# Optimization experiments

Measured on AMD Instinct MI355X. Metric: run time of the kernel, lower is better.

The kernel has to match this reference:

```python
import jax, jax.numpy as jnp
import numpy as np

BLOCK_H, BLOCK_W = 8, 8
IMG_H, IMG_W = 256, 512
NBLOCKS = 256
NSEQ = 256
BATCH = 16
TILES = (IMG_H // BLOCK_H) * (IMG_W // BLOCK_W)  # 2048
TAU = 1.0


def gen_deblocking_lut():
    l = np.zeros((3, 3, 3), np.float32)
    l[2, 0, 0] = 1.0
    l[1, 0, 1] = 1.0; l[2, 0, 1] = 2.0
    l[0, 0, 2] = 1.0; l[1, 0, 2] = 1.0; l[2, 0, 2] = 2.0
    l[1, 1, 0] = 1.0; l[2, 1, 0] = 2.0
    l[0, 1, 1] = 1.0; l[1, 1, 1] = 1.0; l[2, 1, 1] = 2.0
    l[0, 1, 2] = 1.0; l[1, 1, 2] = 2.0; l[2, 1, 2] = 2.0
    l[0, 2, 0] = 1.0; l[1, 2, 0] = 1.0; l[2, 2, 0] = 2.0
    l[0, 2, 1] = 1.0; l[1, 2, 1] = 2.0; l[2, 2, 1] = 2.0
    l[0, 2, 2] = 1.0; l[1, 2, 2] = 2.0; l[2, 2, 2] = 2.0
    return jnp.asarray(l)


def trilinear_interp(lut, x, y, z):
    # lut: (3,3,3); x,y,z: same shape, floats (indices clamped like torch version)
    x0 = jnp.clip(jnp.floor(x), 0, 1).astype(jnp.int32)
    y0 = jnp.clip(jnp.floor(y), 0, 1).astype(jnp.int32)
    z0 = jnp.clip(jnp.floor(z), 0, 1).astype(jnp.int32)
    x1 = jnp.clip(x0 + 1, 0, 2)
    y1 = jnp.clip(y0 + 1, 0, 2)
    z1 = jnp.clip(z0 + 1, 0, 2)
    xd = x - x0.astype(x.dtype)
    yd = y - y0.astype(y.dtype)
    zd = z - z0.astype(z.dtype)
    c000 = lut[x0, y0, z0]; c100 = lut[x1, y0, z0]
    c010 = lut[x0, y1, z0]; c110 = lut[x1, y1, z0]
    c001 = lut[x0, y0, z1]; c101 = lut[x1, y0, z1]
    c011 = lut[x0, y1, z1]; c111 = lut[x1, y1, z1]
    c00 = c000 * (1 - xd) * (1 - yd) + c100 * xd * (1 - yd) + c010 * (1 - xd) * yd + c110 * xd * yd
    c01 = c001 * (1 - xd) * (1 - yd) + c101 * xd * (1 - yd) + c011 * (1 - xd) * yd + c111 * xd * yd
    return c00 * (1 - zd) + c01 * zd


def deblocking_filter(img_raw, lut):
    # Faithful port, including the source quirks: second pass reuses `center`
    # (pre-filter image) in the LUT lookup and shifts along W, not H.
    img = img_raw * 2
    B, C, H, W = img.shape
    xm = jnp.arange(W) % BLOCK_W
    ym = jnp.arange(H) % BLOCK_H
    mask_x = ((xm == 0) | (xm == BLOCK_W - 1)).reshape(1, 1, 1, W)
    mask_y = ((ym == 0) | (ym == BLOCK_H - 1)).reshape(1, 1, H, 1)
    padded = jnp.pad(img, ((0, 0), (0, 0), (1, 1), (1, 1)), mode='edge')
    center = padded[:, :, 1:-1, 1:-1]
    left = padded[:, :, 1:-1, :-2]
    right = padded[:, :, 1:-1, 2:]
    filtered = jnp.where(mask_x, trilinear_interp(lut, center, left, right), center)
    padded2 = jnp.pad(filtered, ((0, 0), (0, 0), (1, 1), (1, 1)), mode='edge')
    center2 = padded2[:, :, 1:-1, 1:-1]
    up = padded2[:, :, 1:-1, :-2]
    down = padded2[:, :, 1:-1, 2:]
    filtered2 = jnp.where(mask_y, trilinear_interp(lut, center, up, down), center2)
    return filtered2 / 2


def setup_inputs() -> dict:
    key = jax.random.key(0)
    k1, k2, k3, k4 = jax.random.split(key, 4)
    sequence = jax.random.normal(k1, (NSEQ, TILES, NBLOCKS), dtype=jnp.float32)
    blocks = jax.random.normal(k2, (NBLOCKS, BLOCK_H, BLOCK_W), dtype=jnp.float32)
    gumbel = jax.random.gumbel(k3, (BATCH, TILES, NBLOCKS), dtype=jnp.float32)
    frame_idxs = jax.random.randint(k4, (BATCH,), 0, NSEQ)
    lut = gen_deblocking_lut()
    return {"sequence": sequence, "blocks": blocks, "lut": lut,
            "gumbel": gumbel, "frame_idxs": frame_idxs}


def reference(sequence, blocks, lut, gumbel, frame_idxs):
    # Training branch: soft gumbel-softmax over the codebook per tile.
    logits = sequence[frame_idxs]                       # [B, T, N]
    block_weights = jax.nn.softmax((logits + gumbel) / TAU, axis=-1)
    block_len = BLOCK_H * BLOCK_W
    # soft codebook lookup, already permuted: [B, block_len, T]
    uf = jnp.einsum('btn,nk->bkt', block_weights, blocks.reshape(NBLOCKS, block_len))
    Hb, Wb = IMG_H // BLOCK_H, IMG_W // BLOCK_W
    # Fold (non-overlapping, stride == kernel)
    rec = uf.reshape(-1, BLOCK_H, BLOCK_W, Hb, Wb)
    rec = rec.transpose(0, 3, 1, 4, 2).reshape(-1, 1, IMG_H, IMG_W)
    return deblocking_filter(rec, lut)
```

## Files before the change

### kernel.cpp

```cpp
#include <hip/hip_runtime.h>


#define NB       256
#define TIL      2048
#define EPITCH   264
#define ROWPITCH 520

typedef short  s8v __attribute__((ext_vector_type(8)));
typedef float  f4v __attribute__((ext_vector_type(4)));

__device__ __forceinline__ unsigned short f2bf(float f) {
    unsigned int u = __float_as_uint(f);
    u += 0x7fffu + ((u >> 16) & 1u);
    return (unsigned short)(u >> 16);
}

__device__ __forceinline__ unsigned int pk2(float a, float b) {
    return (unsigned int)f2bf(a) | ((unsigned int)f2bf(b) << 16);
}

__device__ __forceinline__ float4 ldnt4(const float* p) {
    float4 v;
    v.x = __builtin_nontemporal_load(p + 0);
    v.y = __builtin_nontemporal_load(p + 1);
    v.z = __builtin_nontemporal_load(p + 2);
    v.w = __builtin_nontemporal_load(p + 3);
    return v;
}

__device__ __forceinline__ float trilerp(const float* __restrict__ lutS,
                                         float x, float y, float z) {
    int x0 = (int)fminf(fmaxf(floorf(x), 0.0f), 1.0f);
    int y0 = (int)fminf(fmaxf(floorf(y), 0.0f), 1.0f);
    int z0 = (int)fminf(fmaxf(floorf(z), 0.0f), 1.0f);
    float xd = x - (float)x0;
    float yd = y - (float)y0;
    float zd = z - (float)z0;
    int base = x0 * 9 + y0 * 3 + z0;
    float c000 = lutS[base],     c100 = lutS[base + 9];
    float c010 = lutS[base + 3], c110 = lutS[base + 12];
    float c001 = lutS[base + 1], c101 = lutS[base + 10];
    float c011 = lutS[base + 4], c111 = lutS[base + 13];
    float xm = 1.0f - xd, ym = 1.0f - yd;
    float c00 = c000 * xm * ym + c100 * xd * ym + c010 * xm * yd + c110 * xd * yd;
    float c01 = c001 * xm * ym + c101 * xd * ym + c011 * xm * yd + c111 * xd * yd;
    return c00 * (1.0f - zd) + c01 * zd;
}

__device__ __forceinline__ float fval(const float* __restrict__ row,
                                      const float* __restrict__ fcolr, int x) {
    int x8 = x & 7;
    if (x8 == 0 || x8 == 7) return fcolr[(x >> 3) * 2 + (x8 == 7)];
    return row[x];
}

__global__ __launch_bounds__(256, 2)
void ImageReconstruction_46523085751029_kernel(
        const float* __restrict__ seq,
        const float* __restrict__ blocks,
        const float* __restrict__ lut,
        const float* __restrict__ gumbel,
        const int*   __restrict__ fidx,
        float*       __restrict__ out)
{
    __shared__ __align__(16) unsigned short E[64 * EPITCH];
    __shared__ float lutS[28];

    const int t    = threadIdx.x;
    const int lane = t & 63;
    const int wave = t >> 6;
    const int b    = blockIdx.x >> 5;
    const int hb   = blockIdx.x & 31;

    if (t < 27) lutS[t] = lut[t];

    const int f = fidx[b];
    const float* sp = seq    + (size_t)f * (TIL * NB) + (size_t)hb * (64 * NB);
    const float* gp = gumbel + (size_t)b * (TIL * NB) + (size_t)hb * (64 * NB);

    float4 lq[16], gq[16];
    #pragma unroll
    for (int r = 0; r < 16; ++r) {
        lq[r] = ldnt4(sp + (r * 256 + t) * 4);
        gq[r] = ldnt4(gp + (r * 256 + t) * 4);
    }

    #pragma unroll
    for (int r = 0; r < 16; ++r) {
        int fi = r * 256 + t;
        int tile = fi >> 6;
        int n    = (fi & 63) * 4;
        unsigned int u0 = pk2(__expf(lq[r].x + gq[r].x), __expf(lq[r].y + gq[r].y));
        unsigned int u1 = pk2(__expf(lq[r].z + gq[r].z), __expf(lq[r].w + gq[r].w));
        *(uint2*)&E[tile * EPITCH + n] = make_uint2(u0, u1);
    }

    const int g = lane >> 4;
    const int c = lane & 15;
    const float* bp = blocks + wave * 16 + c;
    s8v bfrag[8];
    #pragma unroll
    for (int ks = 0; ks < 8; ++ks) {
        int k0 = ks * 32 + g * 8;
        unsigned int u[4];
        #pragma unroll
        for (int jj = 0; jj < 4; ++jj)
            u[jj] = pk2(bp[(k0 + 2 * jj) * 64], bp[(k0 + 2 * jj + 1) * 64]);
        int4 iv = make_int4(u[0], u[1], u[2], u[3]);
        bfrag[ks] = __builtin_bit_cast(s8v, iv);
    }
    s8v ones;
    {
        unsigned int uo = (c == 0) ? 0x3F803F80u : 0u;
        int4 iv = make_int4(uo, uo, uo, uo);
        ones = __builtin_bit_cast(s8v, iv);
    }

    __syncthreads();

    f4v acc[4], accd[4];
    #pragma unroll
    for (int mt = 0; mt < 4; ++mt) { acc[mt] = (f4v)0.0f; accd[mt] = (f4v)0.0f; }

    #pragma unroll
    for (int ks = 0; ks < 8; ++ks) {
        #pragma unroll
        for (int mt = 0; mt < 4; ++mt) {
            s8v a = *(const s8v*)&E[(mt * 16 + c) * EPITCH + ks * 32 + g * 8];
            acc[mt]  = __builtin_amdgcn_mfma_f32_16x16x32_bf16(a, bfrag[ks], acc[mt],  0, 0, 0);
            accd[mt] = __builtin_amdgcn_mfma_f32_16x16x32_bf16(a, ones,      accd[mt], 0, 0, 0);
        }
    }

    __syncthreads();

    float* rows_img = (float*)E;
    float* fcol     = (float*)E + 8 * ROWPITCH;

    #pragma unroll
    for (int mt = 0; mt < 4; ++mt) {
        #pragma unroll
        for (int rg = 0; rg < 4; ++rg) {
            float den = __shfl(accd[mt][rg], (lane >> 4) * 16);
            float val = acc[mt][rg] * (2.0f / den);
            int row = mt * 16 + g * 4 + rg;
            int p   = wave * 16 + c;
            int bh  = p >> 3, bw = p & 7;
            rows_img[bh * ROWPITCH + row * 8 + bw] = val;
        }
    }
    __syncthreads();

    #pragma unroll
    for (int it = 0; it < 4; ++it) {
        int idx = it * 256 + t;
        int bh = idx >> 7, ci = idx & 127;
        int w  = (ci >> 1) * 8 + ((ci & 1) ? 7 : 0);
        const float* row = rows_img + bh * ROWPITCH;
        int wm = (w > 0)   ? w - 1 : 0;
        int wp = (w < 511) ? w + 1 : 511;
        fcol[bh * 128 + ci] = trilerp(lutS, row[w], row[wm], row[wp]);
    }
    __syncthreads();

    float* op = out + (size_t)b * (256 * 512) + (size_t)hb * (8 * 512);
    #pragma unroll 2
    for (int it = 0; it < 16; ++it) {
        int pix = it * 256 + t;
        int bh = pix >> 9, w = pix & 511;
        const float* row = rows_img + bh * ROWPITCH;
        const float* fr  = fcol + bh * 128;
        float gv;
        if (bh == 0 || bh == 7) {
            int wm = (w > 0)   ? w - 1 : 0;
            int wp = (w < 511) ? w + 1 : 511;
            gv = trilerp(lutS, row[w], fval(row, fr, wm), fval(row, fr, wp));
        } else {
            gv = fval(row, fr, w);
        }
        __builtin_nontemporal_store(0.5f * gv, op + bh * 512 + w);
    }
}

extern "C" void kernel_launch(void* const* d_in, const int* in_sizes, int n_in,
                              void* d_out, int out_size, void* d_ws, size_t ws_size,
                              hipStream_t stream) {
    const float* seq    = (const float*)d_in[0];
    const float* blocks = (const float*)d_in[1];
    const float* lut    = (const float*)d_in[2];
    const float* gumbel = (const float*)d_in[3];
    const int*   fidx   = (const int*)d_in[4];
    float* out = (float*)d_out;

    dim3 grid(512);
    dim3 block(256);
    ImageReconstruction_46523085751029_kernel<<<grid, block, 0, stream>>>(
        seq, blocks, lut, gumbel, fidx, out);
}
```

Measured before the change: 19.98 us.

## Split fused kernel into matvec and filter kernels via workspace for more parallelism

Splits the single fused kernel into two launches. The first is a softmax-weighted codebook matmul over 2048 blocks of 16 tiles each, which writes the unfiltered image to a workspace buffer. The second runs the deblocking filter over image row-strips. The goal is four times more blocks with less shared memory and fewer registers each, for better occupancy and memory-latency hiding. The cost is an extra global round trip of the 8 MB image plus a second kernel launch, with the old fused kernel kept as a fallback when the workspace is too small.

```diff
diff --git a/kernel.cpp b/kernel.cpp
--- a/kernel.cpp
+++ b/kernel.cpp
@@ -54,45 +54,32 @@
     return row[x];
 }
 
-__global__ __launch_bounds__(256, 2)
-void ImageReconstruction_46523085751029_kernel(
-        const float* __restrict__ seq,
-        const float* __restrict__ blocks,
-        const float* __restrict__ lut,
-        const float* __restrict__ gumbel,
-        const int*   __restrict__ fidx,
-        float*       __restrict__ out)
+__global__ __launch_bounds__(256, 4)
+void IR_matvec_kernel(
+        const float* __restrict__ seq, const float* __restrict__ blocks,
+        const float* __restrict__ gumbel, const int* __restrict__ fidx,
+        float* __restrict__ ws)
 {
-    __shared__ __align__(16) unsigned short E[64 * EPITCH];
-    __shared__ float lutS[28];
+    __shared__ __align__(16) unsigned short E[16 * EPITCH];
 
     const int t    = threadIdx.x;
     const int lane = t & 63;
     const int wave = t >> 6;
-    const int b    = blockIdx.x >> 5;
-    const int hb   = blockIdx.x & 31;
-
-    if (t < 27) lutS[t] = lut[t];
+    const int bid  = blockIdx.x;
+    const int b    = bid >> 7;
+    const int hb   = (bid >> 2) & 31;
+    const int qt   = bid & 3;
 
     const int f = fidx[b];
-    const float* sp = seq    + (size_t)f * (TIL * NB) + (size_t)hb * (64 * NB);
-    const float* gp = gumbel + (size_t)b * (TIL * NB) + (size_t)hb * (64 * NB);
-
-    float4 lq[16], gq[16];
-    #pragma unroll
-    for (int r = 0; r < 16; ++r) {
+    const size_t tbase = (size_t)(hb * 64 + qt * 16) * NB;
+    const float* sp = seq    + (size_t)f * (TIL * NB) + tbase;
+    const float* gp = gumbel + (size_t)b * (TIL * NB) + tbase;
+
+    float4 lq[4], gq[4];
+    #pragma unroll
+    for (int r = 0; r < 4; ++r) {
         lq[r] = ldnt4(sp + (r * 256 + t) * 4);
         gq[r] = ldnt4(gp + (r * 256 + t) * 4);
-    }
-
-    #pragma unroll
-    for (int r = 0; r < 16; ++r) {
-        int fi = r * 256 + t;
-        int tile = fi >> 6;
-        int n    = (fi & 63) * 4;
-        unsigned int u0 = pk2(__expf(lq[r].x + gq[r].x), __expf(lq[r].y + gq[r].y));
-        unsigned int u1 = pk2(__expf(lq[r].z + gq[r].z), __expf(lq[r].w + gq[r].w));
-        *(uint2*)&E[tile * EPITCH + n] = make_uint2(u0, u1);
     }
 
     const int g = lane >> 4;
@@ -116,38 +103,59 @@
         ones = __builtin_bit_cast(s8v, iv);
     }
 
-    __syncthreads();
-
-    f4v acc[4], accd[4];
-    #pragma unroll
-    for (int mt = 0; mt < 4; ++mt) { acc[mt] = (f4v)0.0f; accd[mt] = (f4v)0.0f; }
-
+    #pragma unroll
+    for (int r = 0; r < 4; ++r) {
+        int fi = r * 256 + t;
+        int tile = fi >> 6;
+        int n    = (fi & 63) * 4;
+        unsigned int u0 = pk2(__expf(lq[r].x + gq[r].x), __expf(lq[r].y + gq[r].y));
+        unsigned int u1 = pk2(__expf(lq[r].z + gq[r].z), __expf(lq[r].w + gq[r].w));
+        *(uint2*)&E[tile * EPITCH + n] = make_uint2(u0, u1);
+    }
+    __syncthreads();
+
+    f4v acc = (f4v)0.0f, accd = (f4v)0.0f;
     #pragma unroll
     for (int ks = 0; ks < 8; ++ks) {
-        #pragma unroll
-        for (int mt = 0; mt < 4; ++mt) {
-            s8v a = *(const s8v*)&E[(mt * 16 + c) * EPITCH + ks * 32 + g * 8];
-            acc[mt]  = __builtin_amdgcn_mfma_f32_16x16x32_bf16(a, bfrag[ks], acc[mt],  0, 0, 0);
-            accd[mt] = __builtin_amdgcn_mfma_f32_16x16x32_bf16(a, ones,      accd[mt], 0, 0, 0);
-        }
-    }
-
-    __syncthreads();
-
-    float* rows_img = (float*)E;
-    float* fcol     = (float*)E + 8 * ROWPITCH;
-
-    #pragma unroll
-    for (int mt = 0; mt < 4; ++mt) {
-        #pragma unroll
-        for (int rg = 0; rg < 4; ++rg) {
-            float den = __shfl(accd[mt][rg], (lane >> 4) * 16);
-            float val = acc[mt][rg] * (2.0f / den);
-            int row = mt * 16 + g * 4 + rg;
-            int p   = wave * 16 + c;
-            int bh  = p >> 3, bw = p & 7;
-            rows_img[bh * ROWPITCH + row * 8 + bw] = val;
-        }
+        s8v a = *(const s8v*)&E[c * EPITCH + ks * 32 + g * 8];
+        acc  = __builtin_amdgcn_mfma_f32_16x16x32_bf16(a, bfrag[ks], acc,  0, 0, 0);
+        accd = __builtin_amdgcn_mfma_f32_16x16x32_bf16(a, ones,      accd, 0, 0, 0);
+    }
+
+    float* wp = ws + ((size_t)(b * 32 + hb) * 8) * 512;
+    const int p  = wave * 16 + c;
+    const int bh = p >> 3, bw = p & 7;
+    #pragma unroll
+    for (int rg = 0; rg < 4; ++rg) {
+        float den = __shfl(accd[rg], (lane >> 4) * 16);
+        float val = acc[rg] * (2.0f / den);
+        int tl = g * 4 + rg;
+        int w  = (qt * 16 + tl) * 8 + bw;
+        __builtin_nontemporal_store(val, wp + bh * 512 + w);
+    }
+}
+
+__global__ __launch_bounds__(256, 4)
+void IR_filter_kernel(const float* __restrict__ ws,
+                      const float* __restrict__ lut,
+                      float* __restrict__ out)
+{
+    __shared__ float rows_img[8 * ROWPITCH];
+    __shared__ float fcol[8 * 128];
+    __shared__ float lutS[28];
+
+    const int t = threadIdx.x;
+    if (t < 27) lutS[t] = lut[t];
+
+    const float* ip = ws  + (size_t)blockIdx.x * (8 * 512);
+    float*       op = out + (size_t)blockIdx.x * (8 * 512);
+
+    #pragma unroll
+    for (int r = 0; r < 4; ++r) {
+        int fi = r * 256 + t;
+        float4 v = ldnt4(ip + fi * 4);
+        int bh = fi >> 7, n = (fi & 127) * 4;
+        *(float4*)&rows_img[bh * ROWPITCH + n] = v;
     }
     __syncthreads();
 
@@ -163,7 +171,6 @@
     }
     __syncthreads();
 
-    float* op = out + (size_t)b * (256 * 512) + (size_t)hb * (8 * 512);
     #pragma unroll 2
     for (int it = 0; it < 16; ++it) {
         int pix = it * 256 + t;
@@ -182,6 +189,126 @@
     }
 }
 
+__global__ __launch_bounds__(256, 2)
+void IR_mono_kernel(
+        const float* __restrict__ seq, const float* __restrict__ blocks,
+        const float* __restrict__ lut, const float* __restrict__ gumbel,
+        const int* __restrict__ fidx, float* __restrict__ out)
+{
+    __shared__ __align__(16) unsigned short E[64 * EPITCH];
+    __shared__ float lutS[28];
+
+    const int t    = threadIdx.x;
+    const int lane = t & 63;
+    const int wave = t >> 6;
+    const int b    = blockIdx.x >> 5;
+    const int hb   = blockIdx.x & 31;
+
+    if (t < 27) lutS[t] = lut[t];
+
+    const int f = fidx[b];
+    const float* sp = seq    + (size_t)f * (TIL * NB) + (size_t)hb * (64 * NB);
+    const float* gp = gumbel + (size_t)b * (TIL * NB) + (size_t)hb * (64 * NB);
+
+    float4 lq[16], gq[16];
+    #pragma unroll
+    for (int r = 0; r < 16; ++r) {
+        lq[r] = ldnt4(sp + (r * 256 + t) * 4);
+        gq[r] = ldnt4(gp + (r * 256 + t) * 4);
+    }
+    #pragma unroll
+    for (int r = 0; r < 16; ++r) {
+        int fi = r * 256 + t;
+        int tile = fi >> 6;
+        int n    = (fi & 63) * 4;
+        unsigned int u0 = pk2(__expf(lq[r].x + gq[r].x), __expf(lq[r].y + gq[r].y));
+        unsigned int u1 = pk2(__expf(lq[r].z + gq[r].z), __expf(lq[r].w + gq[r].w));
+        *(uint2*)&E[tile * EPITCH + n] = make_uint2(u0, u1);
+    }
+
+    const int g = lane >> 4;
+    const int c = lane & 15;
+    const float* bp = blocks + wave * 16 + c;
+    s8v bfrag[8];
+    #pragma unroll
+    for (int ks = 0; ks < 8; ++ks) {
+        int k0 = ks * 32 + g * 8;
+        unsigned int u[4];
+        #pragma unroll
+        for (int jj = 0; jj < 4; ++jj)
+            u[jj] = pk2(bp[(k0 + 2 * jj) * 64], bp[(k0 + 2 * jj + 1) * 64]);
+        int4 iv = make_int4(u[0], u[1], u[2], u[3]);
+        bfrag[ks] = __builtin_bit_cast(s8v, iv);
+    }
+    s8v ones;
+    {
+        unsigned int uo = (c == 0) ? 0x3F803F80u : 0u;
+        int4 iv = make_int4(uo, uo, uo, uo);
+        ones = __builtin_bit_cast(s8v, iv);
+    }
+    __syncthreads();
+
+    f4v acc[4], accd[4];
+    #pragma unroll
+    for (int mt = 0; mt < 4; ++mt) { acc[mt] = (f4v)0.0f; accd[mt] = (f4v)0.0f; }
+    #pragma unroll
+    for (int ks = 0; ks < 8; ++ks) {
+        #pragma unroll
+        for (int mt = 0; mt < 4; ++mt) {
+            s8v a = *(const s8v*)&E[(mt * 16 + c) * EPITCH + ks * 32 + g * 8];
+            acc[mt]  = __builtin_amdgcn_mfma_f32_16x16x32_bf16(a, bfrag[ks], acc[mt],  0, 0, 0);
+            accd[mt] = __builtin_amdgcn_mfma_f32_16x16x32_bf16(a, ones,      accd[mt], 0, 0, 0);
+        }
+    }
+    __syncthreads();
+
+    float* rows_img = (float*)E;
+    float* fcol     = (float*)E + 8 * ROWPITCH;
+    #pragma unroll
+    for (int mt = 0; mt < 4; ++mt) {
+        #pragma unroll
+        for (int rg = 0; rg < 4; ++rg) {
+            float den = __shfl(accd[mt][rg], (lane >> 4) * 16);
+            float val = acc[mt][rg] * (2.0f / den);
+            int row = mt * 16 + g * 4 + rg;
+            int p   = wave * 16 + c;
+            int bh  = p >> 3, bw = p & 7;
+            rows_img[bh * ROWPITCH + row * 8 + bw] = val;
+        }
+    }
+    __syncthreads();
+
+    #pragma unroll
+    for (int it = 0; it < 4; ++it) {
+        int idx = it * 256 + t;
+        int bh = idx >> 7, ci = idx & 127;
+        int w  = (ci >> 1) * 8 + ((ci & 1) ? 7 : 0);
+        const float* row = rows_img + bh * ROWPITCH;
+        int wm = (w > 0)   ? w - 1 : 0;
+        int wp = (w < 511) ? w + 1 : 511;
+        fcol[bh * 128 + ci] = trilerp(lutS, row[w], row[wm], row[wp]);
+    }
+    __syncthreads();
+
+    float* op = out + (size_t)blockIdx.x * (8 * 512);
+    #pragma unroll 2
+    for (int it = 0; it < 16; ++it) {
+        int pix = it * 256 + t;
+        int bh = pix >> 9, w = pix & 511;
+        const float* row = rows_img + bh * ROWPITCH;
+        const float* fr  = fcol + bh * 128;
+        float gv;
+        if (bh == 0 || bh == 7) {
+            int wm = (w > 0)   ? w - 1 : 0;
+            int wp = (w < 511) ? w + 1 : 511;
+            gv = trilerp(lutS, row[w], fval(row, fr, wm), fval(row, fr, wp));
+        } else {
+            gv = fval(row, fr, w);
+        }
+        __builtin_nontemporal_store(0.5f * gv, op + bh * 512 + w);
+    }
+}
+
 extern "C" void kernel_launch(void* const* d_in, const int* in_sizes, int n_in,
                               void* d_out, int out_size, void* d_ws, size_t ws_size,
                               hipStream_t stream) {
@@ -192,8 +319,14 @@
     const int*   fidx   = (const int*)d_in[4];
     float* out = (float*)d_out;
 
-    dim3 grid(512);
-    dim3 block(256);
-    ImageReconstruction_46523085751029_kernel<<<grid, block, 0, stream>>>(
-        seq, blocks, lut, gumbel, fidx, out);
-}
+    const size_t need = (size_t)16 * 256 * 512 * sizeof(float);
+    if (ws_size >= need) {
+        float* ws = (float*)d_ws;
+        IR_matvec_kernel<<<dim3(2048), dim3(256), 0, stream>>>(
+            seq, blocks, gumbel, fidx, ws);
+        IR_filter_kernel<<<dim3(512), dim3(256), 0, stream>>>(ws, lut, out);
+    } else {
+        IR_mono_kernel<<<dim3(512), dim3(256), 0, stream>>>(
+            seq, blocks, lut, gumbel, fidx, out);
+    }
+}
```

Result: slower. 33.91 us (+69.7%).
